# Optimization experiments

Measured on AMD Instinct MI355X. Metric: run time of the kernel, lower is better.

Reference implementation:

```python
import jax, jax.numpy as jnp
import numpy as np

# kernel_size=3, dilate=1 -> kernel_sample[3]=[0,1,2,3,4] selects these 5 (dy,dx) offsets
OFFSETS = [(-1, -1), (-1, 0), (-1, 1), (0, -1), (0, 0)]
EPS = 1e-12  # F.normalize default eps


def setup_inputs() -> dict:
    key = jax.random.key(0)
    x = jax.random.normal(key, (16, 192, 64, 64), dtype=jnp.float32)
    return {"x": x}


def reference(x):
    B, C, H, W = x.shape
    # ReplicationPad2d(kernel_size//2 = 1) == edge padding
    xp = jnp.pad(x, ((0, 0), (0, 0), (1, 1), (1, 1)), mode="edge")
    # centers are all interior pixels of the padded map == original pixels
    center = x.reshape(B, C, H * W).transpose(0, 2, 1)  # (B, K, C), K = H*W
    cofe = []
    for dy, dx in OFFSETS:
        side = xp[:, :, 1 + dy:1 + dy + H, 1 + dx:1 + dx + W]
        side = side.reshape(B, C, H * W).transpose(0, 2, 1)  # (B, K, C)
        # sum over K of outer products center_k (x) side_k -> (B, C, C)
        co = jnp.einsum('bkc,bkd->bcd', center, side).reshape(B, C * C)
        cofe.append(co)
    cofe = jnp.stack(cofe, axis=1)  # (B, 5, C*C)
    norm = jnp.linalg.norm(cofe, axis=-1, keepdims=True)
    return cofe / jnp.maximum(norm, EPS)
```

## Files before the change

### kernel.cpp

```cpp
#include <hip/hip_runtime.h>
#include <stdint.h>

#define C_CH 192
#define HW   4096
#define NB   16
#define NO   5
#define ARR_SHORTS 12582912

typedef __attribute__((ext_vector_type(8)))  short short8;
typedef __attribute__((ext_vector_type(16))) float floatx16;

__device__ __forceinline__ unsigned short f2bf(float f) {
    unsigned int u = __float_as_uint(f);
    unsigned int r = (u + 0x7fffu + ((u >> 16) & 1u)) >> 16;
    return (unsigned short)r;
}

__global__ __launch_bounds__(256) void convert_kernel(const float* __restrict__ x,
                                                      unsigned short* __restrict__ xb,
                                                      float* __restrict__ norms) {
    if (blockIdx.x == 0 && threadIdx.x < NB * NO) norms[threadIdx.x] = 0.0f;
    int t   = blockIdx.x * 256 + threadIdx.x;
    int grp = t >> 14;
    int idx = t & 16383;
    int qhi = idx >> 8;
    int cp  = (idx >> 3) & 31;
    int qlo = idx & 7;
    int q   = qhi * 8 + qlo;
    int b   = grp / 6;
    int cb  = grp - b * 6;
    int ch  = cb * 32 + cp;
    int h   = q >> 3;
    int j8  = q & 7;
    int w8  = j8 * 8;

    const float* row = x + (size_t)(b * C_CH + ch) * HW + h * 64;
    const float4* p = (const float4*)(row + w8);
    float4 v0 = p[0], v1 = p[1];
    float prevf = row[j8 ? w8 - 1 : 0];
    float nextf = row[j8 < 7 ? w8 + 8 : 63];

    unsigned short b0 = f2bf(v0.x), b1 = f2bf(v0.y), b2 = f2bf(v0.z), b3 = f2bf(v0.w);
    unsigned short b4 = f2bf(v1.x), b5 = f2bf(v1.y), b6 = f2bf(v1.z), b7 = f2bf(v1.w);
    unsigned short pv = f2bf(prevf), nx = f2bf(nextf);

    size_t o8 = (size_t)grp * 16384 + q * 32 + cp;
    ushort4* dX = (ushort4*)xb + o8 * 2;
    ushort4* dM = (ushort4*)(xb + ARR_SHORTS) + o8 * 2;
    ushort4* dP = (ushort4*)(xb + 2 * ARR_SHORTS) + o8 * 2;
    ushort4 u;
    u.x = b0; u.y = b1; u.z = b2; u.w = b3; dX[0] = u;
    u.x = b4; u.y = b5; u.z = b6; u.w = b7; dX[1] = u;
    u.x = pv; u.y = b0; u.z = b1; u.w = b2; dM[0] = u;
    u.x = b3; u.y = b4; u.z = b5; u.w = b6; dM[1] = u;
    u.x = b1; u.y = b2; u.z = b3; u.w = b4; dP[0] = u;
    u.x = b5; u.y = b6; u.z = b7; u.w = nx; dP[1] = u;
}

__global__ __launch_bounds__(256) void cofe_gemm(const unsigned short* __restrict__ xb,
                                                 float* __restrict__ out,
                                                 float* __restrict__ norms) {
    int blk  = blockIdx.x;
    int work = (blk & 7) * 72 + (blk >> 3);
    int b = work / 36;
    int t = work % 36;
    int cbA = t / 6, cbB = t % 6;
    int c0 = cbA * 32, d0 = cbB * 32;

    int wv   = threadIdx.x >> 6;
    int lane = threadIdx.x & 63;
    int lr   = lane & 31;
    int lo   = lane >> 5;
    int laneoff = lo * 32 + lr;

    const short8* XA = (const short8*)xb + (size_t)(b * 6 + cbA) * 16384;
    const short8* XB = (const short8*)xb + (size_t)(b * 6 + cbB) * 16384;
    const short8* MB = (const short8*)(xb + ARR_SHORTS) + (size_t)(b * 6 + cbB) * 16384;
    const short8* PB = (const short8*)(xb + 2 * ARR_SHORTS) + (size_t)(b * 6 + cbB) * 16384;

    floatx16 acc[5];
    #pragma unroll
    for (int o = 0; o < 5; ++o)
        #pragma unroll
        for (int e = 0; e < 16; ++e)
            acc[o][e] = 0.0f;

    int h0 = wv * 16;
#define FR(row, s) (((row) * 8 + 2 * (s)) * 32 + laneoff)

    #pragma unroll
    for (int s = 0; s < 4; ++s) {
        short8 a[4], bx[3], bm[3], bp[3];
        a[0]  = XA[FR(h0, s)];
        a[1]  = XA[FR(h0 + 1, s)];
        a[2]  = XA[FR(h0 + 2, s)];
        bx[0] = XB[FR(h0, s)];  bm[0] = MB[FR(h0, s)];  bp[0] = PB[FR(h0, s)];
        bx[1] = XB[FR(h0 + 1, s)]; bm[1] = MB[FR(h0 + 1, s)]; bp[1] = PB[FR(h0 + 1, s)];

        if (wv == 0) {
            acc[0] = __builtin_amdgcn_mfma_f32_32x32x16_bf16(a[0], bm[0], acc[0], 0, 0, 0);
            acc[1] = __builtin_amdgcn_mfma_f32_32x32x16_bf16(a[0], bx[0], acc[1], 0, 0, 0);
            acc[2] = __builtin_amdgcn_mfma_f32_32x32x16_bf16(a[0], bp[0], acc[2], 0, 0, 0);
        }

        #pragma unroll
        for (int r = 0; r < 16; ++r) {
            int g   = h0 + r;
            const int ia  = r & 3;
            const int ia1 = (r + 1) & 3;
            const int ipa = (r + 3) & 3;
            const int ib  = r % 3;
            const int ipb = (r + 2) % 3;
            int ga = (g + 3 < 64) ? g + 3 : 63;
            int gb = (g + 2 < 64) ? g + 2 : 63;

            a[ipa]  = XA[FR(ga, s)];
            bx[ipb] = XB[FR(gb, s)];
            bm[ipb] = MB[FR(gb, s)];
            bp[ipb] = PB[FR(gb, s)];

            acc[4] = __builtin_amdgcn_mfma_f32_32x32x16_bf16(a[ia],  bx[ib], acc[4], 0, 0, 0);
            acc[3] = __builtin_amdgcn_mfma_f32_32x32x16_bf16(a[ia],  bm[ib], acc[3], 0, 0, 0);
            if (r < 15 || wv < 3) {
                acc[1] = __builtin_amdgcn_mfma_f32_32x32x16_bf16(a[ia1], bx[ib], acc[1], 0, 0, 0);
                acc[0] = __builtin_amdgcn_mfma_f32_32x32x16_bf16(a[ia1], bm[ib], acc[0], 0, 0, 0);
                acc[2] = __builtin_amdgcn_mfma_f32_32x32x16_bf16(a[ia1], bp[ib], acc[2], 0, 0, 0);
            }
        }
    }
#undef FR

    __shared__ float red[4096];
    __shared__ float wsum[4];
    float4* red4 = (float4*)red;
    size_t obase = (size_t)b * NO * (C_CH * C_CH);
    int tt = threadIdx.x;

    for (int o = 0; o < 5; ++o) {
        __syncthreads();
        #pragma unroll
        for (int reg = 0; reg < 16; ++reg) {
            int row = (reg & 3) + 8 * (reg >> 2) + 4 * lo;
            red[wv * 1024 + row * 32 + lr] = acc[o][reg];
        }
        __syncthreads();
        float4 s  = red4[tt];
        float4 s1 = red4[256 + tt];
        float4 s2 = red4[512 + tt];
        float4 s3 = red4[768 + tt];
        s.x += s1.x + s2.x + s3.x;
        s.y += s1.y + s2.y + s3.y;
        s.z += s1.z + s2.z + s3.z;
        s.w += s1.w + s2.w + s3.w;
        int row = tt >> 3;
        int col = (tt & 7) * 4;
        float* op = out + obase + (size_t)o * (C_CH * C_CH)
                  + (size_t)(c0 + row) * C_CH + d0 + col;
        *(float4*)op = s;

        float ss = s.x * s.x + s.y * s.y + s.z * s.z + s.w * s.w;
        #pragma unroll
        for (int off = 32; off; off >>= 1) ss += __shfl_down(ss, off, 64);
        if (lane == 0) wsum[wv] = ss;
        __syncthreads();
        if (tt == 0) atomicAdd(&norms[b * NO + o], wsum[0] + wsum[1] + wsum[2] + wsum[3]);
    }
}

__global__ __launch_bounds__(256) void scale_kernel(float* __restrict__ out,
                                                    const float* __restrict__ norms) {
    int g  = blockIdx.x * 256 + threadIdx.x;
    int bo = blockIdx.x / 36;
    float s = norms[bo];
    float inv = 1.0f / fmaxf(sqrtf(s), 1e-12f);
    float4 v = ((const float4*)out)[g];
    v.x *= inv; v.y *= inv; v.z *= inv; v.w *= inv;
    ((float4*)out)[g] = v;
}

extern "C" void kernel_launch(void* const* d_in, const int* in_sizes, int n_in,
                              void* d_out, int out_size, void* d_ws, size_t ws_size,
                              hipStream_t stream) {
    const float* x = (const float*)d_in[0];
    float* out = (float*)d_out;
    float* norms = (float*)d_ws;
    unsigned short* xb = (unsigned short*)((char*)d_ws + 512);

    convert_kernel<<<6144, 256, 0, stream>>>(x, xb, norms);
    cofe_gemm<<<576, 256, 0, stream>>>(xb, out, norms);
    scale_kernel<<<2880, 256, 0, stream>>>(out, norms);
}
```

Before: 150.2 us.

## Split GEMM reduction over image rows into chunks with separate reduce kernel

The cofe GEMM now splits the 64 image rows into two chunks when workspace allows, doubling the block count from 576 to 1152 so more CUs stay busy. Each chunk writes partial products to a workspace buffer. A new reduce kernel sums the partials, writes the output and accumulates the squared norms. This costs an extra kernel launch and extra global traffic for writing and re-reading the partial buffers.

Measured after the change: 159.6 us. 6.3% more time.

```diff
diff --git a/kernel.cpp b/kernel.cpp
--- a/kernel.cpp
+++ b/kernel.cpp
@@ -6,6 +6,7 @@
 #define NB   16
 #define NO   5
 #define ARR_SHORTS 12582912
+#define OUTSZ (NB * NO * C_CH * C_CH)
 
 typedef __attribute__((ext_vector_type(8)))  short short8;
 typedef __attribute__((ext_vector_type(16))) float floatx16;
@@ -57,13 +58,17 @@
     u.x = b5; u.y = b6; u.z = b7; u.w = nx; dP[1] = u;
 }
 
+template<int RW>
 __global__ __launch_bounds__(256) void cofe_gemm(const unsigned short* __restrict__ xb,
-                                                 float* __restrict__ out,
-                                                 float* __restrict__ norms) {
+                                                 float* __restrict__ part) {
+    constexpr int NC  = 64 / (4 * RW);
+    constexpr int TPB = NC * 36;
     int blk  = blockIdx.x;
-    int work = (blk & 7) * 72 + (blk >> 3);
-    int b = work / 36;
-    int t = work % 36;
+    int work = (blk & 7) * ((NB * TPB) / 8) + (blk >> 3);
+    int b     = work / TPB;
+    int r0    = work % TPB;
+    int chunk = r0 / 36;
+    int t     = r0 % 36;
     int cbA = t / 6, cbB = t % 6;
     int c0 = cbA * 32, d0 = cbB * 32;
 
@@ -85,7 +90,7 @@
         for (int e = 0; e < 16; ++e)
             acc[o][e] = 0.0f;
 
-    int h0 = wv * 16;
+    int h0 = chunk * (4 * RW) + wv * RW;
 #define FR(row, s) (((row) * 8 + 2 * (s)) * 32 + laneoff)
 
     #pragma unroll
@@ -94,17 +99,17 @@
         a[0]  = XA[FR(h0, s)];
         a[1]  = XA[FR(h0 + 1, s)];
         a[2]  = XA[FR(h0 + 2, s)];
-        bx[0] = XB[FR(h0, s)];  bm[0] = MB[FR(h0, s)];  bp[0] = PB[FR(h0, s)];
+        bx[0] = XB[FR(h0, s)];     bm[0] = MB[FR(h0, s)];     bp[0] = PB[FR(h0, s)];
         bx[1] = XB[FR(h0 + 1, s)]; bm[1] = MB[FR(h0 + 1, s)]; bp[1] = PB[FR(h0 + 1, s)];
 
-        if (wv == 0) {
+        if (h0 == 0) {
             acc[0] = __builtin_amdgcn_mfma_f32_32x32x16_bf16(a[0], bm[0], acc[0], 0, 0, 0);
             acc[1] = __builtin_amdgcn_mfma_f32_32x32x16_bf16(a[0], bx[0], acc[1], 0, 0, 0);
             acc[2] = __builtin_amdgcn_mfma_f32_32x32x16_bf16(a[0], bp[0], acc[2], 0, 0, 0);
         }
 
         #pragma unroll
-        for (int r = 0; r < 16; ++r) {
+        for (int r = 0; r < RW; ++r) {
             int g   = h0 + r;
             const int ia  = r & 3;
             const int ia1 = (r + 1) & 3;
@@ -121,7 +126,7 @@
 
             acc[4] = __builtin_amdgcn_mfma_f32_32x32x16_bf16(a[ia],  bx[ib], acc[4], 0, 0, 0);
             acc[3] = __builtin_amdgcn_mfma_f32_32x32x16_bf16(a[ia],  bm[ib], acc[3], 0, 0, 0);
-            if (r < 15 || wv < 3) {
+            if (r < RW - 1 || g < 63) {
                 acc[1] = __builtin_amdgcn_mfma_f32_32x32x16_bf16(a[ia1], bx[ib], acc[1], 0, 0, 0);
                 acc[0] = __builtin_amdgcn_mfma_f32_32x32x16_bf16(a[ia1], bm[ib], acc[0], 0, 0, 0);
                 acc[2] = __builtin_amdgcn_mfma_f32_32x32x16_bf16(a[ia1], bp[ib], acc[2], 0, 0, 0);
@@ -131,9 +136,8 @@
 #undef FR
 
     __shared__ float red[4096];
-    __shared__ float wsum[4];
     float4* red4 = (float4*)red;
-    size_t obase = (size_t)b * NO * (C_CH * C_CH);
+    size_t pbase = ((size_t)chunk * (NB * NO) + b * NO) * (C_CH * C_CH);
     int tt = threadIdx.x;
 
     for (int o = 0; o < 5; ++o) {
@@ -154,17 +158,32 @@
         s.w += s1.w + s2.w + s3.w;
         int row = tt >> 3;
         int col = (tt & 7) * 4;
-        float* op = out + obase + (size_t)o * (C_CH * C_CH)
+        float* op = part + pbase + (size_t)o * (C_CH * C_CH)
                   + (size_t)(c0 + row) * C_CH + d0 + col;
         *(float4*)op = s;
-
-        float ss = s.x * s.x + s.y * s.y + s.z * s.z + s.w * s.w;
-        #pragma unroll
-        for (int off = 32; off; off >>= 1) ss += __shfl_down(ss, off, 64);
-        if (lane == 0) wsum[wv] = ss;
-        __syncthreads();
-        if (tt == 0) atomicAdd(&norms[b * NO + o], wsum[0] + wsum[1] + wsum[2] + wsum[3]);
-    }
+    }
+}
+
+__global__ __launch_bounds__(256) void reduce_kernel(const float* __restrict__ part,
+                                                     float* __restrict__ out,
+                                                     float* __restrict__ norms,
+                                                     int nchunk) {
+    int g  = blockIdx.x * 256 + threadIdx.x;
+    int bo = blockIdx.x / 36;
+    float4 s = ((const float4*)part)[g];
+    for (int c = 1; c < nchunk; ++c) {
+        float4 v = ((const float4*)part)[(size_t)c * (OUTSZ / 4) + g];
+        s.x += v.x; s.y += v.y; s.z += v.z; s.w += v.w;
+    }
+    ((float4*)out)[g] = s;
+    float ss = s.x * s.x + s.y * s.y + s.z * s.z + s.w * s.w;
+    #pragma unroll
+    for (int off = 32; off; off >>= 1) ss += __shfl_down(ss, off, 64);
+    __shared__ float wsum[4];
+    if ((threadIdx.x & 63) == 0) wsum[threadIdx.x >> 6] = ss;
+    __syncthreads();
+    if (threadIdx.x == 0)
+        atomicAdd(&norms[bo], wsum[0] + wsum[1] + wsum[2] + wsum[3]);
 }
 
 __global__ __launch_bounds__(256) void scale_kernel(float* __restrict__ out,
@@ -185,8 +204,21 @@
     float* out = (float*)d_out;
     float* norms = (float*)d_ws;
     unsigned short* xb = (unsigned short*)((char*)d_ws + 512);
+    const size_t base = 512 + 3 * (size_t)ARR_SHORTS * 2;
+    float* part = (float*)((char*)d_ws + base);
+    const size_t chunk_bytes = (size_t)OUTSZ * 4;
 
     convert_kernel<<<6144, 256, 0, stream>>>(x, xb, norms);
-    cofe_gemm<<<576, 256, 0, stream>>>(xb, out, norms);
+
+    int nchunk;
+    if (ws_size >= base + 2 * chunk_bytes) {
+        nchunk = 2;
+        cofe_gemm<8><<<NB * 36 * 2, 256, 0, stream>>>(xb, part);
+    } else {
+        nchunk = 1;
+        cofe_gemm<16><<<NB * 36, 256, 0, stream>>>(xb, part);
+    }
+
+    reduce_kernel<<<2880, 256, 0, stream>>>(part, out, norms, nchunk);
     scale_kernel<<<2880, 256, 0, stream>>>(out, norms);
 }
```
